# Kernel optimization log

Measured on AMD Instinct MI355X. Metric: run time of the kernel, lower is better.

## Reference

```python
import jax, jax.numpy as jnp
import numpy as np

N_NODES = 100000
N_EDGES = 600000
D = 128          # embedding_dim == hidden_dim
OUT = 128        # output_dim
L = 5            # number of GINConv layers


def setup_inputs() -> dict:
    key = jax.random.key(0)
    ks = jax.random.split(key, 9)
    return {
        "x": jax.random.randint(ks[0], (N_NODES,), 0, N_NODES),
        "edge_index": jax.random.randint(ks[1], (2, N_EDGES), 0, N_NODES),
        "emb": jax.random.normal(ks[2], (N_NODES, D), dtype=jnp.float32) * 0.02,
        "Wa": jax.random.normal(ks[3], (L, D, D), dtype=jnp.float32) * 0.05,
        "ba": jnp.zeros((L, D), dtype=jnp.float32),
        "Wb": jax.random.normal(ks[4], (L, D, D), dtype=jnp.float32) * 0.05,
        "bb": jnp.zeros((L, D), dtype=jnp.float32),
        "Wlin": jax.random.normal(ks[5], (D, OUT), dtype=jnp.float32) * 0.05,
        "blin": jnp.zeros((OUT,), dtype=jnp.float32),
    }


def reference(x, edge_index, emb, Wa, ba, Wb, bb, Wlin, blin):
    src, dst = edge_index[0], edge_index[1]
    h = emb[x]  # [N, D] embedding lookup
    for l in range(L):
        # GINConv with eps=0: mlp((1+eps)*x_i + sum_{j->i} x_j)
        agg = jax.ops.segment_sum(h[src], dst, num_segments=N_NODES)  # [N, D]
        z = h + agg
        z = jax.nn.relu(z @ Wa[l] + ba[l])  # MLP hidden
        z = z @ Wb[l] + bb[l]               # MLP out
        h = jax.nn.relu(z)                  # outer F.relu in forward
    pooled = jnp.sum(h, axis=0, keepdims=True)  # global_add_pool, batch=None -> [1, D]
    return pooled @ Wlin + blin                  # [1, OUT]
```

## Files before the change

### kernel.cpp

```cpp
#include <hip/hip_runtime.h>

#define D 128
#define NLAYERS 5

using short8  = __attribute__((ext_vector_type(8))) short;
using short4v = __attribute__((ext_vector_type(4))) short;
using floatx4 = __attribute__((ext_vector_type(4))) float;
using floatx2 = __attribute__((ext_vector_type(2))) float;

__device__ __forceinline__ unsigned bf16_rne(float x) {
    unsigned u = __float_as_uint(x);
    return (u + 0x7fffu + ((u >> 16) & 1u)) >> 16;
}
__device__ __forceinline__ float bf16_to_f32(short s) {
    return __uint_as_float(((unsigned)(unsigned short)s) << 16);
}

#define HSCALE 16.0f
#define HSCALE_INV 0.0625f

__global__ void prepA_kernel(const int* __restrict__ x, const float* __restrict__ emb,
                             const float* __restrict__ Wa, const float* __restrict__ Wb,
                             const int* __restrict__ edst,
                             unsigned char* __restrict__ H0, short* __restrict__ wt,
                             int* __restrict__ deg,
                             int n_nodes, int n_edges) {
    const int gtid = blockIdx.x * 256 + threadIdx.x;
    const int gsz  = gridDim.x * 256;
    for (int g = gtid; g < 2 * NLAYERS * D * D; g += gsz) {
        int mat = g >> 14, idx = g & 16383;
        int n = idx >> 7, k = idx & 127;
        const float* W = (mat & 1) ? (Wb + (size_t)(mat >> 1) * D * D)
                                   : (Wa + (size_t)(mat >> 1) * D * D);
        wt[g] = (short)bf16_rne(W[k * D + n]);
    }
    for (int t = gtid; t < n_nodes * 32; t += gsz) {
        int node = t >> 5, lane = t & 31;
        int s = x[node];
        const float4 v = *reinterpret_cast<const float4*>(emb + (size_t)s * D + lane * 4);
        int w = __builtin_amdgcn_cvt_pk_fp8_f32(v.x * HSCALE, v.y * HSCALE, 0, false);
        w = __builtin_amdgcn_cvt_pk_fp8_f32(v.z * HSCALE, v.w * HSCALE, w, true);
        reinterpret_cast<unsigned int*>(H0)[(size_t)node * 32 + lane] = (unsigned int)w;
    }
    for (int e = gtid; e < n_edges; e += gsz) atomicAdd(&deg[edst[e]], 1);
}

#define SCAN_TILE 1024
__global__ void scan_sums_kernel(const int* __restrict__ deg, int* __restrict__ bsums, int n) {
    __shared__ int red[256];
    int base = blockIdx.x * SCAN_TILE + threadIdx.x * 4;
    int s = 0;
    #pragma unroll
    for (int j = 0; j < 4; j++) {
        int i = base + j;
        if (i < n) s += deg[i];
    }
    red[threadIdx.x] = s;
    __syncthreads();
    for (int off = 128; off > 0; off >>= 1) {
        if (threadIdx.x < off) red[threadIdx.x] += red[threadIdx.x + off];
        __syncthreads();
    }
    if (threadIdx.x == 0) bsums[blockIdx.x] = red[0];
}

__global__ void scan_bsums_kernel(int* __restrict__ bsums, int nblocks) {
    __shared__ int sdata[256];
    int carry = 0;
    for (int base = 0; base < nblocks; base += 256) {
        int i = base + threadIdx.x;
        int v = (i < nblocks) ? bsums[i] : 0;
        sdata[threadIdx.x] = v;
        __syncthreads();
        for (int off = 1; off < 256; off <<= 1) {
            int t = (threadIdx.x >= off) ? sdata[threadIdx.x - off] : 0;
            __syncthreads();
            sdata[threadIdx.x] += t;
            __syncthreads();
        }
        int incl = sdata[threadIdx.x];
        if (i < nblocks) bsums[i] = carry + incl - v;
        carry += sdata[255];
        __syncthreads();
    }
}

__global__ void scan_final_kernel(const int* __restrict__ deg, const int* __restrict__ bsums,
                                  int* __restrict__ offsets, int* __restrict__ cursor, int n) {
    __shared__ int sdata[256];
    int base = blockIdx.x * SCAN_TILE + threadIdx.x * 4;
    int v[4];
    int s = 0;
    #pragma unroll
    for (int j = 0; j < 4; j++) {
        int i = base + j;
        v[j] = (i < n) ? deg[i] : 0;
        s += v[j];
    }
    sdata[threadIdx.x] = s;
    __syncthreads();
    for (int off = 1; off < 256; off <<= 1) {
        int t = (threadIdx.x >= off) ? sdata[threadIdx.x - off] : 0;
        __syncthreads();
        sdata[threadIdx.x] += t;
        __syncthreads();
    }
    int excl = sdata[threadIdx.x] - s + bsums[blockIdx.x];
    #pragma unroll
    for (int j = 0; j < 4; j++) {
        int i = base + j;
        if (i <= n) offsets[i] = excl;
        if (i < n) cursor[i] = excl;
        excl += v[j];
    }
}

__global__ void fill_kernel(const int* __restrict__ esrc, const int* __restrict__ edst,
                            int* __restrict__ cursor, int* __restrict__ csr_src, int n_edges) {
    int e = blockIdx.x * 256 + threadIdx.x;
    if (e >= n_edges) return;
    int pos = atomicAdd(&cursor[edst[e]], 1);
    csr_src[pos] = esrc[e];
}

__device__ __forceinline__ void agg_row(const int* __restrict__ offsets,
                                        const int* __restrict__ csr_src,
                                        const unsigned char* __restrict__ h_in,
                                        int gr, int l8, float* acc) {
    {
        uint4 w = *reinterpret_cast<const uint4*>(h_in + (size_t)gr * D + l8 * 16);
        unsigned int wd[4] = {w.x, w.y, w.z, w.w};
        #pragma unroll
        for (int k = 0; k < 4; k++) {
            floatx2 lo = __builtin_amdgcn_cvt_pk_f32_fp8((int)wd[k], false);
            floatx2 hi = __builtin_amdgcn_cvt_pk_f32_fp8((int)wd[k], true);
            acc[4 * k]     = lo[0]; acc[4 * k + 1] = lo[1];
            acc[4 * k + 2] = hi[0]; acc[4 * k + 3] = hi[1];
        }
    }
    int e   = offsets[gr];
    int end = offsets[gr + 1];
    for (; e + 3 < end; e += 4) {
        int sA = csr_src[e];
        int sB = csr_src[e + 1];
        int sC = csr_src[e + 2];
        int sD = csr_src[e + 3];
        uint4 wA = *reinterpret_cast<const uint4*>(h_in + (size_t)sA * D + l8 * 16);
        uint4 wB = *reinterpret_cast<const uint4*>(h_in + (size_t)sB * D + l8 * 16);
        uint4 wC = *reinterpret_cast<const uint4*>(h_in + (size_t)sC * D + l8 * 16);
        uint4 wD = *reinterpret_cast<const uint4*>(h_in + (size_t)sD * D + l8 * 16);
        unsigned int da[4] = {wA.x, wA.y, wA.z, wA.w};
        unsigned int db[4] = {wB.x, wB.y, wB.z, wB.w};
        unsigned int dc[4] = {wC.x, wC.y, wC.z, wC.w};
        unsigned int dd[4] = {wD.x, wD.y, wD.z, wD.w};
        #pragma unroll
        for (int k = 0; k < 4; k++) {
            floatx2 alo = __builtin_amdgcn_cvt_pk_f32_fp8((int)da[k], false);
            floatx2 ahi = __builtin_amdgcn_cvt_pk_f32_fp8((int)da[k], true);
            floatx2 blo = __builtin_amdgcn_cvt_pk_f32_fp8((int)db[k], false);
            floatx2 bhi = __builtin_amdgcn_cvt_pk_f32_fp8((int)db[k], true);
            floatx2 clo = __builtin_amdgcn_cvt_pk_f32_fp8((int)dc[k], false);
            floatx2 chi = __builtin_amdgcn_cvt_pk_f32_fp8((int)dc[k], true);
            floatx2 dlo = __builtin_amdgcn_cvt_pk_f32_fp8((int)dd[k], false);
            floatx2 dhi = __builtin_amdgcn_cvt_pk_f32_fp8((int)dd[k], true);
            acc[4 * k]     += (alo[0] + blo[0]) + (clo[0] + dlo[0]);
            acc[4 * k + 1] += (alo[1] + blo[1]) + (clo[1] + dlo[1]);
            acc[4 * k + 2] += (ahi[0] + bhi[0]) + (chi[0] + dhi[0]);
            acc[4 * k + 3] += (ahi[1] + bhi[1]) + (chi[1] + dhi[1]);
        }
    }
    for (; e < end; e++) {
        int sA = csr_src[e];
        uint4 wA = *reinterpret_cast<const uint4*>(h_in + (size_t)sA * D + l8 * 16);
        unsigned int da[4] = {wA.x, wA.y, wA.z, wA.w};
        #pragma unroll
        for (int k = 0; k < 4; k++) {
            floatx2 alo = __builtin_amdgcn_cvt_pk_f32_fp8((int)da[k], false);
            floatx2 ahi = __builtin_amdgcn_cvt_pk_f32_fp8((int)da[k], true);
            acc[4 * k]     += alo[0];
            acc[4 * k + 1] += alo[1];
            acc[4 * k + 2] += ahi[0];
            acc[4 * k + 3] += ahi[1];
        }
    }
}

__global__ __launch_bounds__(1024, 8) void layer_kernel(
        const int* __restrict__ offsets, const int* __restrict__ csr_src,
        const unsigned char* __restrict__ h_in, const short* __restrict__ wta,
        const short* __restrict__ wtb, const float* __restrict__ ba,
        const float* __restrict__ bb, unsigned char* __restrict__ h_out,
        float* __restrict__ pooled_accum, int n_rows) {
    __shared__ __align__(16) short zsh[128 * 128];
    __shared__ __align__(16) short wsh[128 * 128];

    const int tid  = threadIdx.x;
    const int row0 = blockIdx.x * 128;

    #pragma unroll
    for (int i = 0; i < 2; i++) {
        int g = i * 1024 + tid;
        int n = g >> 4, c = g & 15;
        int off = (n * 16 + (c ^ (n & 15))) * 8;
        *reinterpret_cast<short8*>(&wsh[off]) =
            *reinterpret_cast<const short8*>(wta + n * D + c * 8);
    }

    {
        const int r  = tid >> 3;
        const int l8 = tid & 7;
        const int gr = row0 + r;
        float acc[16];
        if (gr < n_rows) {
            agg_row(offsets, csr_src, h_in, gr, l8, acc);
        } else {
            #pragma unroll
            for (int j = 0; j < 16; j++) acc[j] = 0.f;
        }
        short8 o0, o1;
        #pragma unroll
        for (int j = 0; j < 8; j++) {
            o0[j] = (short)bf16_rne(acc[j] * HSCALE_INV);
            o1[j] = (short)bf16_rne(acc[8 + j] * HSCALE_INV);
        }
        const int c0i = 2 * l8, c1i = 2 * l8 + 1;
        *reinterpret_cast<short8*>(&zsh[(r * 16 + (c0i ^ (r & 15))) * 8]) = o0;
        *reinterpret_cast<short8*>(&zsh[(r * 16 + (c1i ^ (r & 15))) * 8]) = o1;
    }
    __syncthreads();

    const int lane = tid & 63;
    const int wave = tid >> 6;
    const int wr   = wave >> 1;
    const int wc   = wave & 1;
    const int lm   = lane & 15;
    const int quad = lane >> 4;

    floatx4 acc1[4];
    #pragma unroll
    for (int cs = 0; cs < 4; cs++) acc1[cs] = floatx4{0.f, 0.f, 0.f, 0.f};
    {
        const int r = wr * 16 + lm;
        #pragma unroll
        for (int ks = 0; ks < 4; ks++) {
            const int c = ks * 4 + quad;
            short8 av = *reinterpret_cast<const short8*>(&zsh[(r * 16 + (c ^ (r & 15))) * 8]);
            #pragma unroll
            for (int cs = 0; cs < 4; cs++) {
                int nn = wc * 64 + cs * 16 + lm;
                short8 bv = *reinterpret_cast<const short8*>(&wsh[(nn * 16 + (c ^ (nn & 15))) * 8]);
                acc1[cs] = __builtin_amdgcn_mfma_f32_16x16x32_bf16(av, bv, acc1[cs], 0, 0, 0);
            }
        }
    }
    __syncthreads();

    #pragma unroll
    for (int i = 0; i < 2; i++) {
        int g = i * 1024 + tid;
        int n = g >> 4, c = g & 15;
        int off = (n * 16 + (c ^ (n & 15))) * 8;
        *reinterpret_cast<short8*>(&wsh[off]) =
            *reinterpret_cast<const short8*>(wtb + n * D + c * 8);
    }

    #pragma unroll
    for (int cs = 0; cs < 4; cs++) {
        int col = wc * 64 + cs * 16 + lm;
        float bva = ba[col];
        int cj = col >> 3, ci = col & 7;
        #pragma unroll
        for (int reg = 0; reg < 4; reg++) {
            int r = wr * 16 + quad * 4 + reg;
            float v = fmaxf(acc1[cs][reg] + bva, 0.f);
            zsh[(r * 16 + (cj ^ (r & 15))) * 8 + ci] = (short)bf16_rne(v);
        }
    }
    __syncthreads();

    floatx4 acc2[4];
    #pragma unroll
    for (int cs = 0; cs < 4; cs++) acc2[cs] = floatx4{0.f, 0.f, 0.f, 0.f};
    {
        const int r = wr * 16 + lm;
        #pragma unroll
        for (int ks = 0; ks < 4; ks++) {
            const int c = ks * 4 + quad;
            short8 av = *reinterpret_cast<const short8*>(&zsh[(r * 16 + (c ^ (r & 15))) * 8]);
            #pragma unroll
            for (int cs = 0; cs < 4; cs++) {
                int nn = wc * 64 + cs * 16 + lm;
                short8 bv = *reinterpret_cast<const short8*>(&wsh[(nn * 16 + (c ^ (nn & 15))) * 8]);
                acc2[cs] = __builtin_amdgcn_mfma_f32_16x16x32_bf16(av, bv, acc2[cs], 0, 0, 0);
            }
        }
    }

    float psum[4];
    #pragma unroll
    for (int cs = 0; cs < 4; cs++) {
        int col = wc * 64 + cs * 16 + lm;
        float bvb = bb[col];
        float s = 0.f;
        #pragma unroll
        for (int reg = 0; reg < 4; reg++) {
            int r = row0 + wr * 16 + quad * 4 + reg;
            if (r < n_rows) {
                float v = fmaxf(acc2[cs][reg] + bvb, 0.f);
                if (h_out != nullptr) {
                    float sv = v * HSCALE;
                    int pw = __builtin_amdgcn_cvt_pk_fp8_f32(sv, sv, 0, false);
                    h_out[(size_t)r * D + col] = (unsigned char)(pw & 0xff);
                }
                s += v;
            }
        }
        psum[cs] = s;
    }

    if (pooled_accum != nullptr) {
        __syncthreads();
        float* part = (float*)zsh;
        #pragma unroll
        for (int cs = 0; cs < 4; cs++)
            part[(wr * 4 + quad) * 128 + wc * 64 + cs * 16 + lm] = psum[cs];
        __syncthreads();
        if (tid < 128) {
            float s = 0.f;
            #pragma unroll
            for (int g = 0; g < 32; g++) s += part[g * 128 + tid];
            atomicAdd(&pooled_accum[tid], s);
        }
    }
}

__global__ void final_kernel(const float* __restrict__ pooled, const float* __restrict__ Wlin,
                             const float* __restrict__ blin, float* __restrict__ out) {
    const int j = threadIdx.x;
    __shared__ float p[D];
    p[j] = pooled[j];
    __syncthreads();
    float s = blin[j];
    #pragma unroll 8
    for (int k = 0; k < D; k++) s += p[k] * Wlin[k * D + j];
    out[j] = s;
}

extern "C" void kernel_launch(void* const* d_in, const int* in_sizes, int n_in,
                              void* d_out, int out_size, void* d_ws, size_t ws_size,
                              hipStream_t stream) {
    const int*   x    = (const int*)d_in[0];
    const int*   ei   = (const int*)d_in[1];
    const float* emb  = (const float*)d_in[2];
    const float* Wa   = (const float*)d_in[3];
    const float* ba   = (const float*)d_in[4];
    const float* Wb   = (const float*)d_in[5];
    const float* bb   = (const float*)d_in[6];
    const float* Wlin = (const float*)d_in[7];
    const float* blin = (const float*)d_in[8];
    float* out = (float*)d_out;

    const int N = in_sizes[0];
    const int E = in_sizes[1] / 2;
    const int* esrc = ei;
    const int* edst = ei + E;

    unsigned char* H0 = (unsigned char*)d_ws;
    unsigned char* H1 = H0 + (size_t)N * D;
    float* pooled = (float*)(H1 + (size_t)N * D);
    int* deg     = (int*)(pooled + 128);
    int* offsets = deg + N;
    int* cursor  = offsets + (N + 1);
    int* bsums   = cursor + N;
    int* csr_src = bsums + 4096;
    uintptr_t wt_addr = ((uintptr_t)(csr_src + E) + 15) & ~(uintptr_t)15;
    short* wt = (short*)wt_addr;

    const int scan_blocks = (N + 1 + SCAN_TILE - 1) / SCAN_TILE;

    hipMemsetAsync(pooled, 0, (size_t)(128 + N) * sizeof(int), stream);

    prepA_kernel<<<1024, 256, 0, stream>>>(x, emb, Wa, Wb, edst, H0, wt, deg, N, E);
    scan_sums_kernel<<<scan_blocks, 256, 0, stream>>>(deg, bsums, N);
    scan_bsums_kernel<<<1, 256, 0, stream>>>(bsums, scan_blocks);
    scan_final_kernel<<<scan_blocks, 256, 0, stream>>>(deg, bsums, offsets, cursor, N);
    fill_kernel<<<(E + 255) / 256, 256, 0, stream>>>(esrc, edst, cursor, csr_src, E);

    const int layer_blocks = (N + 127) / 128;
    unsigned char* hin = H0; unsigned char* hout = H1;
    for (int l = 0; l < NLAYERS; l++) {
        const bool last = (l == NLAYERS - 1);
        float* pacc = last ? pooled : nullptr;
        unsigned char* hdst = last ? nullptr : hout;
        layer_kernel<<<layer_blocks, 1024, 0, stream>>>(
            offsets, csr_src, hin,
            wt + (size_t)(2 * l) * D * D, wt + (size_t)(2 * l + 1) * D * D,
            ba + (size_t)l * D, bb + (size_t)l * D, hdst, pacc, N);
        unsigned char* tmp = hin; hin = hout; hout = tmp;
    }

    final_kernel<<<1, 128, 0, stream>>>(pooled, Wlin, blin, out);
}
```

Before: 355.6 us.

## Bucket CSR edges by source range and convert embedding table before gather

Edges are now binned into NB=4 source-range buckets per destination, so each row's aggregation walks neighbours bucket by bucket. This orders the gathers more locally across the wavefronts running at the same time. The embedding table is converted to fp8 once, with a contiguous pass, and a separate kernel then gathers it by x. Together these are meant to improve cache locality in the irregular gathers. In exchange, the scan covers four times as many entries, there is an extra kernel launch and more workspace, and the inner loop is unrolled by 2 instead of 4, leaving fewer loads in flight.

New measurement: 395.6 us. +11.3%, slower.

```diff
diff --git a/kernel.cpp b/kernel.cpp
--- a/kernel.cpp
+++ b/kernel.cpp
@@ -2,6 +2,7 @@
 
 #define D 128
 #define NLAYERS 5
+#define NB 4
 
 using short8  = __attribute__((ext_vector_type(8))) short;
 using short4v = __attribute__((ext_vector_type(4))) short;
@@ -19,12 +20,12 @@
 #define HSCALE 16.0f
 #define HSCALE_INV 0.0625f
 
-__global__ void prepA_kernel(const int* __restrict__ x, const float* __restrict__ emb,
-                             const float* __restrict__ Wa, const float* __restrict__ Wb,
-                             const int* __restrict__ edst,
-                             unsigned char* __restrict__ H0, short* __restrict__ wt,
-                             int* __restrict__ deg,
-                             int n_nodes, int n_edges) {
+__global__ void conv_hist_kernel(const float* __restrict__ emb,
+                                 const float* __restrict__ Wa, const float* __restrict__ Wb,
+                                 const int* __restrict__ esrc, const int* __restrict__ edst,
+                                 unsigned char* __restrict__ emb8, short* __restrict__ wt,
+                                 int* __restrict__ deg,
+                                 int n_nodes, int n_edges, int rpb) {
     const int gtid = blockIdx.x * 256 + threadIdx.x;
     const int gsz  = gridDim.x * 256;
     for (int g = gtid; g < 2 * NLAYERS * D * D; g += gsz) {
@@ -35,14 +36,25 @@
         wt[g] = (short)bf16_rne(W[k * D + n]);
     }
     for (int t = gtid; t < n_nodes * 32; t += gsz) {
-        int node = t >> 5, lane = t & 31;
-        int s = x[node];
-        const float4 v = *reinterpret_cast<const float4*>(emb + (size_t)s * D + lane * 4);
+        const float4 v = *reinterpret_cast<const float4*>(emb + (size_t)t * 4);
         int w = __builtin_amdgcn_cvt_pk_fp8_f32(v.x * HSCALE, v.y * HSCALE, 0, false);
         w = __builtin_amdgcn_cvt_pk_fp8_f32(v.z * HSCALE, v.w * HSCALE, w, true);
-        reinterpret_cast<unsigned int*>(H0)[(size_t)node * 32 + lane] = (unsigned int)w;
-    }
-    for (int e = gtid; e < n_edges; e += gsz) atomicAdd(&deg[edst[e]], 1);
+        reinterpret_cast<unsigned int*>(emb8)[t] = (unsigned int)w;
+    }
+    for (int e = gtid; e < n_edges; e += gsz) {
+        int b = esrc[e] / rpb;
+        atomicAdd(&deg[b * n_nodes + edst[e]], 1);
+    }
+}
+
+__global__ void gather_kernel(const int* __restrict__ x, const unsigned char* __restrict__ emb8,
+                              unsigned char* __restrict__ H0, int n_nodes) {
+    const int t = blockIdx.x * 256 + threadIdx.x;
+    if (t >= n_nodes * 8) return;
+    const int node = t >> 3, l8 = t & 7;
+    const int s = x[node];
+    uint4 w = *reinterpret_cast<const uint4*>(emb8 + (size_t)s * D + l8 * 16);
+    *reinterpret_cast<uint4*>(H0 + (size_t)node * D + l8 * 16) = w;
 }
 
 #define SCAN_TILE 1024
@@ -116,17 +128,20 @@
 }
 
 __global__ void fill_kernel(const int* __restrict__ esrc, const int* __restrict__ edst,
-                            int* __restrict__ cursor, int* __restrict__ csr_src, int n_edges) {
+                            int* __restrict__ cursor, int* __restrict__ csr_src,
+                            int n_nodes, int n_edges, int rpb) {
     int e = blockIdx.x * 256 + threadIdx.x;
     if (e >= n_edges) return;
-    int pos = atomicAdd(&cursor[edst[e]], 1);
-    csr_src[pos] = esrc[e];
-}
-
-__device__ __forceinline__ void agg_row(const int* __restrict__ offsets,
-                                        const int* __restrict__ csr_src,
-                                        const unsigned char* __restrict__ h_in,
-                                        int gr, int l8, float* acc) {
+    int src = esrc[e];
+    int b = src / rpb;
+    int pos = atomicAdd(&cursor[b * n_nodes + edst[e]], 1);
+    csr_src[pos] = src;
+}
+
+__device__ __forceinline__ void agg_row_blocked(const int* __restrict__ offsets,
+                                                const int* __restrict__ csr_src,
+                                                const unsigned char* __restrict__ h_in,
+                                                int gr, int l8, int n_rows, float* acc) {
     {
         uint4 w = *reinterpret_cast<const uint4*>(h_in + (size_t)gr * D + l8 * 16);
         unsigned int wd[4] = {w.x, w.y, w.z, w.w};
@@ -138,49 +153,43 @@
             acc[4 * k + 2] = hi[0]; acc[4 * k + 3] = hi[1];
         }
     }
-    int e   = offsets[gr];
-    int end = offsets[gr + 1];
-    for (; e + 3 < end; e += 4) {
-        int sA = csr_src[e];
-        int sB = csr_src[e + 1];
-        int sC = csr_src[e + 2];
-        int sD = csr_src[e + 3];
-        uint4 wA = *reinterpret_cast<const uint4*>(h_in + (size_t)sA * D + l8 * 16);
-        uint4 wB = *reinterpret_cast<const uint4*>(h_in + (size_t)sB * D + l8 * 16);
-        uint4 wC = *reinterpret_cast<const uint4*>(h_in + (size_t)sC * D + l8 * 16);
-        uint4 wD = *reinterpret_cast<const uint4*>(h_in + (size_t)sD * D + l8 * 16);
-        unsigned int da[4] = {wA.x, wA.y, wA.z, wA.w};
-        unsigned int db[4] = {wB.x, wB.y, wB.z, wB.w};
-        unsigned int dc[4] = {wC.x, wC.y, wC.z, wC.w};
-        unsigned int dd[4] = {wD.x, wD.y, wD.z, wD.w};
-        #pragma unroll
-        for (int k = 0; k < 4; k++) {
-            floatx2 alo = __builtin_amdgcn_cvt_pk_f32_fp8((int)da[k], false);
-            floatx2 ahi = __builtin_amdgcn_cvt_pk_f32_fp8((int)da[k], true);
-            floatx2 blo = __builtin_amdgcn_cvt_pk_f32_fp8((int)db[k], false);
-            floatx2 bhi = __builtin_amdgcn_cvt_pk_f32_fp8((int)db[k], true);
-            floatx2 clo = __builtin_amdgcn_cvt_pk_f32_fp8((int)dc[k], false);
-            floatx2 chi = __builtin_amdgcn_cvt_pk_f32_fp8((int)dc[k], true);
-            floatx2 dlo = __builtin_amdgcn_cvt_pk_f32_fp8((int)dd[k], false);
-            floatx2 dhi = __builtin_amdgcn_cvt_pk_f32_fp8((int)dd[k], true);
-            acc[4 * k]     += (alo[0] + blo[0]) + (clo[0] + dlo[0]);
-            acc[4 * k + 1] += (alo[1] + blo[1]) + (clo[1] + dlo[1]);
-            acc[4 * k + 2] += (ahi[0] + bhi[0]) + (chi[0] + dhi[0]);
-            acc[4 * k + 3] += (ahi[1] + bhi[1]) + (chi[1] + dhi[1]);
-        }
-    }
-    for (; e < end; e++) {
-        int sA = csr_src[e];
-        uint4 wA = *reinterpret_cast<const uint4*>(h_in + (size_t)sA * D + l8 * 16);
-        unsigned int da[4] = {wA.x, wA.y, wA.z, wA.w};
-        #pragma unroll
-        for (int k = 0; k < 4; k++) {
-            floatx2 alo = __builtin_amdgcn_cvt_pk_f32_fp8((int)da[k], false);
-            floatx2 ahi = __builtin_amdgcn_cvt_pk_f32_fp8((int)da[k], true);
-            acc[4 * k]     += alo[0];
-            acc[4 * k + 1] += alo[1];
-            acc[4 * k + 2] += ahi[0];
-            acc[4 * k + 3] += ahi[1];
+    #pragma unroll
+    for (int b = 0; b < NB; b++) {
+        const int g = b * n_rows + gr;
+        int e   = offsets[g];
+        int end = offsets[g + 1];
+        for (; e + 1 < end; e += 2) {
+            int sA = csr_src[e];
+            int sB = csr_src[e + 1];
+            uint4 wA = *reinterpret_cast<const uint4*>(h_in + (size_t)sA * D + l8 * 16);
+            uint4 wB = *reinterpret_cast<const uint4*>(h_in + (size_t)sB * D + l8 * 16);
+            unsigned int da[4] = {wA.x, wA.y, wA.z, wA.w};
+            unsigned int db[4] = {wB.x, wB.y, wB.z, wB.w};
+            #pragma unroll
+            for (int k = 0; k < 4; k++) {
+                floatx2 alo = __builtin_amdgcn_cvt_pk_f32_fp8((int)da[k], false);
+                floatx2 ahi = __builtin_amdgcn_cvt_pk_f32_fp8((int)da[k], true);
+                floatx2 blo = __builtin_amdgcn_cvt_pk_f32_fp8((int)db[k], false);
+                floatx2 bhi = __builtin_amdgcn_cvt_pk_f32_fp8((int)db[k], true);
+                acc[4 * k]     += (alo[0] + blo[0]);
+                acc[4 * k + 1] += (alo[1] + blo[1]);
+                acc[4 * k + 2] += (ahi[0] + bhi[0]);
+                acc[4 * k + 3] += (ahi[1] + bhi[1]);
+            }
+        }
+        if (e < end) {
+            int sA = csr_src[e];
+            uint4 wA = *reinterpret_cast<const uint4*>(h_in + (size_t)sA * D + l8 * 16);
+            unsigned int da[4] = {wA.x, wA.y, wA.z, wA.w};
+            #pragma unroll
+            for (int k = 0; k < 4; k++) {
+                floatx2 alo = __builtin_amdgcn_cvt_pk_f32_fp8((int)da[k], false);
+                floatx2 ahi = __builtin_amdgcn_cvt_pk_f32_fp8((int)da[k], true);
+                acc[4 * k]     += alo[0];
+                acc[4 * k + 1] += alo[1];
+                acc[4 * k + 2] += ahi[0];
+                acc[4 * k + 3] += ahi[1];
+            }
         }
     }
 }
@@ -212,7 +221,7 @@
         const int gr = row0 + r;
         float acc[16];
         if (gr < n_rows) {
-            agg_row(offsets, csr_src, h_in, gr, l8, acc);
+            agg_row_blocked(offsets, csr_src, h_in, gr, l8, n_rows, acc);
         } else {
             #pragma unroll
             for (int j = 0; j < 16; j++) acc[j] = 0.f;
@@ -364,27 +373,31 @@
     const int E = in_sizes[1] / 2;
     const int* esrc = ei;
     const int* edst = ei + E;
-
-    unsigned char* H0 = (unsigned char*)d_ws;
-    unsigned char* H1 = H0 + (size_t)N * D;
-    float* pooled = (float*)(H1 + (size_t)N * D);
+    const int rpb = (N + NB - 1) / NB;
+
+    unsigned char* H0   = (unsigned char*)d_ws;
+    unsigned char* H1   = H0 + (size_t)N * D;
+    unsigned char* emb8 = H1 + (size_t)N * D;
+    float* pooled = (float*)(emb8 + (size_t)N * D);
     int* deg     = (int*)(pooled + 128);
-    int* offsets = deg + N;
-    int* cursor  = offsets + (N + 1);
-    int* bsums   = cursor + N;
+    int* offsets = deg + (size_t)NB * N;
+    int* cursor  = offsets + ((size_t)NB * N + 1);
+    int* bsums   = cursor + (size_t)NB * N;
     int* csr_src = bsums + 4096;
     uintptr_t wt_addr = ((uintptr_t)(csr_src + E) + 15) & ~(uintptr_t)15;
     short* wt = (short*)wt_addr;
 
-    const int scan_blocks = (N + 1 + SCAN_TILE - 1) / SCAN_TILE;
-
-    hipMemsetAsync(pooled, 0, (size_t)(128 + N) * sizeof(int), stream);
-
-    prepA_kernel<<<1024, 256, 0, stream>>>(x, emb, Wa, Wb, edst, H0, wt, deg, N, E);
-    scan_sums_kernel<<<scan_blocks, 256, 0, stream>>>(deg, bsums, N);
+    const int nscan = NB * N;
+    const int scan_blocks = (nscan + 1 + SCAN_TILE - 1) / SCAN_TILE;
+
+    hipMemsetAsync(pooled, 0, (size_t)(128 + NB * N) * sizeof(int), stream);
+
+    conv_hist_kernel<<<1024, 256, 0, stream>>>(emb, Wa, Wb, esrc, edst, emb8, wt, deg, N, E, rpb);
+    scan_sums_kernel<<<scan_blocks, 256, 0, stream>>>(deg, bsums, nscan);
     scan_bsums_kernel<<<1, 256, 0, stream>>>(bsums, scan_blocks);
-    scan_final_kernel<<<scan_blocks, 256, 0, stream>>>(deg, bsums, offsets, cursor, N);
-    fill_kernel<<<(E + 255) / 256, 256, 0, stream>>>(esrc, edst, cursor, csr_src, E);
+    scan_final_kernel<<<scan_blocks, 256, 0, stream>>>(deg, bsums, offsets, cursor, nscan);
+    fill_kernel<<<(E + 255) / 256, 256, 0, stream>>>(esrc, edst, cursor, csr_src, N, E, rpb);
+    gather_kernel<<<(N * 8 + 255) / 256, 256, 0, stream>>>(x, emb8, H0, N);
 
     const int layer_blocks = (N + 127) / 128;
     unsigned char* hin = H0; unsigned char* hout = H1;
```
